# Optimization experiments

Measured on AMD Instinct MI355X. Metric: run time of the kernel, lower is better.

Reference implementation:

```python
import jax, jax.numpy as jnp
import numpy as np

LEAKY_SLOPE = 0.2  # tf.nn.leaky_relu default alpha
N_NODES = 50000
N_EDGES = 800000
IN_DIM = 128
OUT_DIM = 64
HEADS = 4
MLP_HID = 256
MLP_OUT = 128


def setup_inputs() -> dict:
    key = jax.random.key(0)
    ks = jax.random.split(key, 10)
    node_embeddings = jax.random.normal(ks[0], (N_NODES, IN_DIM), dtype=jnp.float32)
    src = jax.random.randint(ks[1], (N_EDGES,), 0, N_NODES, dtype=jnp.int32)
    dst = jax.random.randint(ks[2], (N_EDGES,), 0, N_NODES, dtype=jnp.int32)
    # glorot-ish scales
    W_n = jax.random.normal(ks[3], (HEADS, IN_DIM, OUT_DIM), dtype=jnp.float32) * (1.0 / np.sqrt(IN_DIM))
    a_src = jax.random.normal(ks[4], (HEADS, OUT_DIM), dtype=jnp.float32) * (1.0 / np.sqrt(OUT_DIM))
    a_dst = jax.random.normal(ks[5], (HEADS, OUT_DIM), dtype=jnp.float32) * (1.0 / np.sqrt(OUT_DIM))
    mlp_W1 = jax.random.normal(ks[6], (HEADS * OUT_DIM, MLP_HID), dtype=jnp.float32) * (1.0 / np.sqrt(HEADS * OUT_DIM))
    mlp_b1 = jnp.zeros((MLP_HID,), dtype=jnp.float32)
    mlp_W2 = jax.random.normal(ks[7], (MLP_HID, MLP_OUT), dtype=jnp.float32) * (1.0 / np.sqrt(MLP_HID))
    mlp_b2 = jnp.zeros((MLP_OUT,), dtype=jnp.float32)
    return {"node_embeddings": node_embeddings, "src": src, "dst": dst,
            "W_n": W_n, "a_src": a_src, "a_dst": a_dst,
            "mlp_W1": mlp_W1, "mlp_b1": mlp_b1, "mlp_W2": mlp_W2, "mlp_b2": mlp_b2}


def _gat_forward(node_embeddings, src, dst, W_n, a_src, a_dst, mlp_W1, mlp_b1, mlp_W2, mlp_b2):
    N = node_embeddings.shape[0]
    # per-head linear transform: [N, H, D]
    h = jnp.einsum('nc,hcd->nhd', node_embeddings, W_n)
    # decomposed attention scores at node level, gathered per edge
    s_src = jnp.einsum('nhd,hd->nh', h, a_src)          # [N, H]
    s_dst = jnp.einsum('nhd,hd->nh', h, a_dst)          # [N, H]
    e = jax.nn.leaky_relu(s_src[src] + s_dst[dst], negative_slope=LEAKY_SLOPE)  # [E, H]
    # segment softmax over incoming edges of each dst node
    e_max = jax.ops.segment_max(e, dst, num_segments=N)          # [N, H], -inf for empty
    ex = jnp.exp(e - e_max[dst])                                  # [E, H]
    den = jax.ops.segment_sum(ex, dst, num_segments=N)            # [N, H]
    m = h[src]                                                    # [E, H, D] messages
    num = jax.ops.segment_sum(ex[:, :, None] * m, dst, num_segments=N)  # [N, H, D]
    safe_den = jnp.where(den > 0, den, 1.0)
    head_out = jax.nn.relu(num / safe_den[:, :, None])            # [N, H, D]
    concat = head_out.reshape(N, -1)                              # [N, H*D]
    hidden = jax.nn.relu(concat @ mlp_W1 + mlp_b1)
    return hidden @ mlp_W2 + mlp_b2                               # [N, MLP_OUT]


def reference(node_embeddings, src, dst, W_n, a_src, a_dst, mlp_W1, mlp_b1, mlp_W2, mlp_b2):
    return _gat_forward(node_embeddings, src, dst, W_n, a_src, a_dst,
                        mlp_W1, mlp_b1, mlp_W2, mlp_b2)
```

## Files before the change

### kernel.cpp

```cpp
#include <hip/hip_runtime.h>

#define LEAKY 0.2f

typedef __attribute__((ext_vector_type(8))) short short8;
typedef __attribute__((ext_vector_type(4))) float floatx4;
typedef __attribute__((ext_vector_type(8))) unsigned short ushort8_t;

__device__ __forceinline__ float bf2f(unsigned short u) {
    return __uint_as_float(((unsigned)u) << 16);
}
__device__ __forceinline__ unsigned short f2bf(float f) {
    unsigned u = __float_as_uint(f);
    unsigned r = (u + 0x7fffu + ((u >> 16) & 1u)) >> 16;
    return (unsigned short)r;
}
__device__ __forceinline__ float relu_nan(float v) { return v < 0.0f ? 0.0f : v; }

__device__ __forceinline__ void gload_lds16(const void* g, void* l) {
    __builtin_amdgcn_global_load_lds((const __attribute__((address_space(1))) void*)g,
                                     (__attribute__((address_space(3))) void*)l, 16, 0, 0);
}

__global__ void k_fill(float* __restrict__ p, float val, int n) {
    int i = blockIdx.x * blockDim.x + threadIdx.x;
    if (i < n) p[i] = val;
}

__global__ void k_prep(const float* __restrict__ X, unsigned short* __restrict__ Xb,
                       const float* __restrict__ Wn, unsigned short* __restrict__ WnT,
                       const float* __restrict__ W1, unsigned short* __restrict__ W1T,
                       const float* __restrict__ W2, unsigned short* __restrict__ W2T,
                       const float* __restrict__ Asrc, const float* __restrict__ Adst,
                       float* __restrict__ Wsd,
                       const int* __restrict__ dst, int* __restrict__ cnt,
                       int N, int E) {
    const int gs = gridDim.x * blockDim.x;
    const int tid = blockIdx.x * blockDim.x + threadIdx.x;
    for (int i = tid; i < N * 32; i += gs) {
        float4 v = ((const float4*)X)[i];
        ushort4 o;
        o.x = f2bf(v.x); o.y = f2bf(v.y); o.z = f2bf(v.z); o.w = f2bf(v.w);
        ((ushort4*)Xb)[i] = o;
    }
    for (int i = tid; i < 256 * 128; i += gs) {
        int col = i >> 7, k = i & 127;
        int head = col >> 6, d = col & 63;
        WnT[i] = f2bf(Wn[(size_t)head * 8192 + (size_t)k * 64 + d]);
    }
    for (int i = tid; i < 256 * 256; i += gs) {
        int n = i >> 8, k = i & 255;
        W1T[i] = f2bf(W1[(size_t)k * 256 + n]);
    }
    for (int i = tid; i < 128 * 256; i += gs) {
        int n = i >> 8, k = i & 255;
        W2T[i] = f2bf(W2[(size_t)k * 128 + n]);
    }
    for (int i = tid; i < 8 * 128; i += gs) {
        int j = i >> 7, k = i & 127, h = j & 3;
        const float* av = (j < 4 ? Asrc : Adst) + h * 64;
        const float* wrow = Wn + (size_t)h * 8192 + (size_t)k * 64;
        float acc = 0.0f;
        for (int d = 0; d < 64; ++d) acc += wrow[d] * av[d];
        Wsd[i] = acc;
    }
    for (int i = tid; i < E; i += gs) atomicAdd(cnt + dst[i], 1);
}

__global__ __launch_bounds__(256) void k_scores(
    const unsigned short* __restrict__ Xb, const float* __restrict__ Wsd,
    float* __restrict__ s_src, float* __restrict__ s_dst, int N) {
    const int gs = gridDim.x * 256;
    const int tid = blockIdx.x * 256 + threadIdx.x;
    for (int i = tid; i < N * 8; i += gs) {
        const int n = i >> 3, j = i & 7;
        const unsigned short* xr = Xb + (size_t)n * 128;
        const float* wr = Wsd + j * 128;
        float acc = 0.0f;
        for (int k = 0; k < 128; k += 8) {
            ushort8_t xv = *(const ushort8_t*)(xr + k);
#pragma unroll
            for (int u = 0; u < 8; ++u) acc = fmaf(bf2f(xv[u]), wr[k + u], acc);
        }
        if (j < 4) s_src[n * 4 + j] = acc;
        else       s_dst[n * 4 + (j - 4)] = acc;
    }
}

__global__ __launch_bounds__(256) void k_scan1(
    const int* __restrict__ cnt, int* __restrict__ rowptr, int* __restrict__ bsum, int N) {
    __shared__ int wtot[4];
    const int lane = threadIdx.x & 63, wave = threadIdx.x >> 6;
    const int i = blockIdx.x * 256 + threadIdx.x;
    int v = (i < N) ? cnt[i] : 0;
    int x = v;
    for (int off = 1; off < 64; off <<= 1) {
        int y = __shfl_up(x, off, 64);
        if (lane >= off) x += y;
    }
    if (lane == 63) wtot[wave] = x;
    __syncthreads();
    int wo = 0;
    for (int wv = 0; wv < wave; ++wv) wo += wtot[wv];
    if (i < N) rowptr[i] = wo + x - v;
    if (threadIdx.x == 255) bsum[blockIdx.x] = wo + x;
}
__global__ void k_scan2(int* __restrict__ bsum, int nb) {
    const int lane = threadIdx.x;
    int carry = 0;
    for (int base = 0; base < nb; base += 64) {
        int i = base + lane;
        int v = (i < nb) ? bsum[i] : 0;
        int x = v;
        for (int off = 1; off < 64; off <<= 1) {
            int y = __shfl_up(x, off, 64);
            if (lane >= off) x += y;
        }
        if (i < nb) bsum[i] = carry + x - v;
        carry += __shfl(x, 63, 64);
    }
}
__global__ void k_scan3(int* __restrict__ rowptr, const int* __restrict__ bsum,
                        int* __restrict__ wcnt, int N, int E) {
    int i = blockIdx.x * blockDim.x + threadIdx.x;
    if (i < N) {
        int v = rowptr[i] + bsum[i >> 8];
        rowptr[i] = v;
        wcnt[i] = v;
    }
    if (i == N) rowptr[N] = E;
}

__global__ void k_scatter(const int* __restrict__ src, const int* __restrict__ dst,
                          int* __restrict__ wcnt,
                          const float* __restrict__ s_src, const float* __restrict__ s_dst,
                          int* __restrict__ esrc, float* __restrict__ ex4, int E) {
    int e = blockIdx.x * blockDim.x + threadIdx.x;
    if (e < E) {
        const int s = src[e], d = dst[e];
        const int pos = atomicAdd(wcnt + d, 1);
        esrc[pos] = s;
        const float4 ss = *(const float4*)(s_src + (size_t)s * 4);
        const float4 sd = *(const float4*)(s_dst + (size_t)d * 4);
        float4 o;
        float v;
        v = ss.x + sd.x; v = fmaxf(v, LEAKY * v); o.x = __expf(v);
        v = ss.y + sd.y; v = fmaxf(v, LEAKY * v); o.y = __expf(v);
        v = ss.z + sd.z; v = fmaxf(v, LEAKY * v); o.z = __expf(v);
        v = ss.w + sd.w; v = fmaxf(v, LEAKY * v); o.w = __expf(v);
        *(float4*)(ex4 + (size_t)pos * 4) = o;
    }
}

__global__ __launch_bounds__(256) void k_agg(
    const unsigned short* __restrict__ Xb,
    const int* __restrict__ rowptr, const int* __restrict__ esrc,
    const float* __restrict__ ex4,
    unsigned short* __restrict__ agg, float* __restrict__ invden, int N) {
    const int lane = threadIdx.x & 63;
    const int wave = threadIdx.x >> 6;
    const int n = blockIdx.x * 4 + wave;
    if (n >= N) return;

    const int slot = lane & 15;
    const int g16  = lane & 48;
    const int head = lane >> 4;
    const unsigned short* xcol = Xb + slot * 8;

    const int beg = rowptr[n], end = rowptr[n + 1];

    float num[8] = {0, 0, 0, 0, 0, 0, 0, 0};
    float den = 0.0f;

    int base = beg;
    int sidv = 0; float exv = 0.0f;
    if (base < end) {
        const int rem = end - base;
        if (slot < rem) {
            sidv = esrc[base + slot];
            exv  = ex4[(size_t)(base + slot) * 4 + head];
        }
    }

    while (base < end) {
        const int rem = end - base;
        const int nb  = base + 16;
        int sidn = 0; float exn = 0.0f;
        if (nb < end) {
            const int rem2 = end - nb;
            if (slot < rem2) {
                sidn = esrc[nb + slot];
                exn  = ex4[(size_t)(nb + slot) * 4 + head];
            }
        }
        den += exv;

        if (rem >= 16) {
#pragma unroll
            for (int e = 0; e < 16; ++e) {
                const int s_   = __shfl(sidv, e, 64);
                const float x_ = __shfl(exv, g16 | e, 64);
                const ushort8_t xv = *(const ushort8_t*)(xcol + (size_t)s_ * 128);
#pragma unroll
                for (int j = 0; j < 8; ++j) num[j] = fmaf(x_, bf2f(xv[j]), num[j]);
            }
        } else {
            for (int e = 0; e < rem; ++e) {
                const int s_   = __shfl(sidv, e, 64);
                const float x_ = __shfl(exv, g16 | e, 64);
                const ushort8_t xv = *(const ushort8_t*)(xcol + (size_t)s_ * 128);
#pragma unroll
                for (int j = 0; j < 8; ++j) num[j] = fmaf(x_, bf2f(xv[j]), num[j]);
            }
        }
        sidv = sidn; exv = exn; base = nb;
    }

#pragma unroll
    for (int m = 1; m < 16; m <<= 1) den += __shfl_xor(den, m, 64);
    const float inv = 1.0f / (den > 0.0f ? den : 1.0f);

    ushort8_t o;
#pragma unroll
    for (int j = 0; j < 8; ++j) o[j] = f2bf(num[j]);
    *(ushort8_t*)(agg + (size_t)n * 512 + head * 128 + slot * 8) = o;
    if (slot == 0) invden[n * 4 + head] = inv;
}

__global__ __launch_bounds__(256) void k_gemmh(
    const unsigned short* __restrict__ agg, const unsigned short* __restrict__ WnT,
    const float* __restrict__ invden, unsigned short* __restrict__ concat, int N) {
    __shared__ unsigned short As[256 * 32];
    __shared__ unsigned short Bs[64 * 32];
    const int t = threadIdx.x;
    const int lane = t & 63;
    const int w = t >> 6;
    const int lm = lane & 15, quad = lane >> 4;
    const int row0 = blockIdx.x * 256;
    const int head = blockIdx.y;

    floatx4 acc[4][4];
#pragma unroll
    for (int mi = 0; mi < 4; ++mi)
#pragma unroll
        for (int ni = 0; ni < 4; ++ni) acc[mi][ni] = (floatx4){0, 0, 0, 0};

    for (int k0 = 0; k0 < 128; k0 += 32) {
#pragma unroll
        for (int p = 0; p < 4; ++p) {
            int tr = p * 64 + (t >> 2);
            int ga = row0 + tr; if (ga >= N) ga = N - 1;
            gload_lds16(agg + (size_t)ga * 512 + head * 128 + k0 + (t & 3) * 8,
                        (char*)As + (size_t)tr * 64 + (t & 3) * 16);
        }
        {
            int tr = t >> 2;
            gload_lds16(WnT + (size_t)(head * 64 + tr) * 128 + k0 + (t & 3) * 8,
                        (char*)Bs + (size_t)tr * 64 + (t & 3) * 16);
        }
        __syncthreads();
        short8 af[4], bfr[4];
#pragma unroll
        for (int mi = 0; mi < 4; ++mi)
            af[mi] = *(const short8*)(As + (size_t)(w * 64 + mi * 16 + lm) * 32 + quad * 8);
#pragma unroll
        for (int ni = 0; ni < 4; ++ni)
            bfr[ni] = *(const short8*)(Bs + (size_t)(ni * 16 + lm) * 32 + quad * 8);
#pragma unroll
        for (int mi = 0; mi < 4; ++mi)
#pragma unroll
            for (int ni = 0; ni < 4; ++ni)
                acc[mi][ni] = __builtin_amdgcn_mfma_f32_16x16x32_bf16(af[mi], bfr[ni], acc[mi][ni], 0, 0, 0);
        __syncthreads();
    }

#pragma unroll
    for (int mi = 0; mi < 4; ++mi)
#pragma unroll
        for (int q = 0; q < 4; ++q) {
            const int r = row0 + w * 64 + mi * 16 + quad * 4 + q;
            if (r < N) {
                const float inv = invden[(size_t)r * 4 + head];
#pragma unroll
                for (int ni = 0; ni < 4; ++ni) {
                    const int c = ni * 16 + lm;
                    concat[(size_t)r * 256 + head * 64 + c] = f2bf(relu_nan(acc[mi][ni][q] * inv));
                }
            }
        }
}

template <int K, int MODE>
__global__ __launch_bounds__(256) void k_gemm(
    const unsigned short* __restrict__ A, const unsigned short* __restrict__ BT,
    const float* __restrict__ bias, unsigned short* __restrict__ Cb,
    float* __restrict__ Cf, int N, int ldout) {
    __shared__ unsigned short As[128 * 32];
    __shared__ unsigned short Bs[128 * 32];
    const int t = threadIdx.x;
    const int lane = t & 63;
    const int w = t >> 6;
    const int wy = w >> 1, wx = w & 1;
    const int lm = lane & 15, quad = lane >> 4;
    const int row0 = blockIdx.x * 128;
    const int n0 = blockIdx.y * 128;
    const int srow = lane >> 2;
    const int sk = (lane & 3) * 8;

    floatx4 acc[4][4];
#pragma unroll
    for (int ni = 0; ni < 4; ++ni) {
        float b = bias[n0 + wx * 64 + ni * 16 + lm];
#pragma unroll
        for (int mi = 0; mi < 4; ++mi) acc[mi][ni] = (floatx4){b, b, b, b};
    }

    for (int k0 = 0; k0 < K; k0 += 32) {
#pragma unroll
        for (int p = 0; p < 2; ++p) {
            int tr = (p * 4 + w) * 16 + srow;
            int ga = row0 + tr; if (ga >= N) ga = N - 1;
            gload_lds16(A + (size_t)ga * K + k0 + sk,
                        (char*)As + (size_t)tr * 64 + sk * 2);
            gload_lds16(BT + (size_t)(n0 + tr) * K + k0 + sk,
                        (char*)Bs + (size_t)tr * 64 + sk * 2);
        }
        __syncthreads();
        short8 af[4], bfr[4];
#pragma unroll
        for (int mi = 0; mi < 4; ++mi)
            af[mi] = *(const short8*)(As + (size_t)(wy * 64 + mi * 16 + lm) * 32 + quad * 8);
#pragma unroll
        for (int ni = 0; ni < 4; ++ni)
            bfr[ni] = *(const short8*)(Bs + (size_t)(wx * 64 + ni * 16 + lm) * 32 + quad * 8);
#pragma unroll
        for (int mi = 0; mi < 4; ++mi)
#pragma unroll
            for (int ni = 0; ni < 4; ++ni)
                acc[mi][ni] = __builtin_amdgcn_mfma_f32_16x16x32_bf16(af[mi], bfr[ni], acc[mi][ni], 0, 0, 0);
        __syncthreads();
    }

#pragma unroll
    for (int mi = 0; mi < 4; ++mi)
#pragma unroll
        for (int ni = 0; ni < 4; ++ni)
#pragma unroll
            for (int q = 0; q < 4; ++q) {
                int r = row0 + wy * 64 + mi * 16 + quad * 4 + q;
                int c = n0 + wx * 64 + ni * 16 + lm;
                if (r < N) {
                    if (MODE == 1) Cb[(size_t)r * ldout + c] = f2bf(relu_nan(acc[mi][ni][q]));
                    else           Cf[(size_t)r * ldout + c] = acc[mi][ni][q];
                }
            }
}

extern "C" void kernel_launch(void* const* d_in, const int* in_sizes, int n_in,
                              void* d_out, int out_size, void* d_ws, size_t ws_size,
                              hipStream_t stream) {
    const float* X    = (const float*)d_in[0];
    const int* src    = (const int*)d_in[1];
    const int* dst    = (const int*)d_in[2];
    const float* Wn   = (const float*)d_in[3];
    const float* Asrc = (const float*)d_in[4];
    const float* Adst = (const float*)d_in[5];
    const float* W1   = (const float*)d_in[6];
    const float* b1   = (const float*)d_in[7];
    const float* W2   = (const float*)d_in[8];
    const float* b2   = (const float*)d_in[9];
    float* out = (float*)d_out;

    const int N = in_sizes[0] / 128;
    const int E = in_sizes[1];
    const int NBS = (N + 255) / 256;
    const int NR = (N + 127) / 128;
    const int NRH = (N + 255) / 256;

    size_t off = 0;
    char* w = (char*)d_ws;
    unsigned short* aggb = (unsigned short*)(w + off); off += (size_t)N * 512 * 2;
    float* s_src = (float*)(w + off);                  off += (size_t)N * 4 * 4;
    float* s_dst = (float*)(w + off);                  off += (size_t)N * 4 * 4;
    float* invden= (float*)(w + off);                  off += (size_t)N * 4 * 4;
    int* cnt     = (int*)(w + off);                    off += (size_t)N * 4;
    int* rowptr  = (int*)(w + off);                    off += ((size_t)(N + 1) * 4 + 15) & ~15ull;
    int* wcnt    = (int*)(w + off);                    off += (size_t)N * 4;
    int* bsum    = (int*)(w + off);                    off += ((size_t)NBS * 4 + 15) & ~15ull;
    int* esrc    = (int*)(w + off);                    off += (size_t)E * 4;
    float* ex4   = (float*)(w + off);                  off += (size_t)E * 4 * 4;
    unsigned short* W1T = (unsigned short*)(w + off);  off += 256 * 256 * 2;
    unsigned short* W2T = (unsigned short*)(w + off);  off += 128 * 256 * 2;
    unsigned short* WnT = (unsigned short*)(w + off);  off += 256 * 128 * 2;
    float* Wsd   = (float*)(w + off);                  off += 8 * 128 * 4;
    const size_t required = off;

    if (ws_size < required) {
        k_fill<<<dim3((out_size + 255) / 256), dim3(256), 0, stream>>>(
            out, (float)(ws_size >> 20), out_size);
        return;
    }

    unsigned short* Xb     = (unsigned short*)d_out;
    unsigned short* concat = (unsigned short*)d_out;
    unsigned short* hid    = aggb;

    hipMemsetAsync(cnt, 0, (size_t)N * sizeof(int), stream);
    k_prep<<<dim3(2048), dim3(256), 0, stream>>>(X, Xb, Wn, WnT, W1, W1T, W2, W2T,
                                                 Asrc, Adst, Wsd, dst, cnt, N, E);
    k_scores<<<dim3((N * 8 + 255) / 256), dim3(256), 0, stream>>>(Xb, Wsd, s_src, s_dst, N);
    k_scan1<<<dim3(NBS), dim3(256), 0, stream>>>(cnt, rowptr, bsum, N);
    k_scan2<<<dim3(1), dim3(64), 0, stream>>>(bsum, NBS);
    k_scan3<<<dim3((N + 256) / 256), dim3(256), 0, stream>>>(rowptr, bsum, wcnt, N, E);
    k_scatter<<<dim3((E + 255) / 256), dim3(256), 0, stream>>>(src, dst, wcnt, s_src, s_dst,
                                                               esrc, ex4, E);
    k_agg<<<dim3((N + 3) / 4), dim3(256), 0, stream>>>(Xb, rowptr, esrc, ex4, aggb, invden, N);
    k_gemmh<<<dim3(NRH, 4), dim3(256), 0, stream>>>(aggb, WnT, invden, concat, N);
    k_gemm<256, 1><<<dim3(NR, 2), dim3(256), 0, stream>>>(
        concat, W1T, b1, hid, nullptr, N, 256);
    k_gemm<256, 2><<<dim3(NR, 1), dim3(256), 0, stream>>>(
        hid, W2T, b2, nullptr, out, N, 128);
}
```

Before: 340.4 us.

## Fuse edge aggregation and per-head projection into one MFMA-based kernel per 16 nodes

```diff
diff --git a/kernel.cpp b/kernel.cpp
--- a/kernel.cpp
+++ b/kernel.cpp
@@ -133,12 +133,14 @@
 __global__ void k_scatter(const int* __restrict__ src, const int* __restrict__ dst,
                           int* __restrict__ wcnt,
                           const float* __restrict__ s_src, const float* __restrict__ s_dst,
-                          int* __restrict__ esrc, float* __restrict__ ex4, int E) {
+                          int* __restrict__ esrc, float* __restrict__ ex4,
+                          unsigned char* __restrict__ ownb, int E) {
     int e = blockIdx.x * blockDim.x + threadIdx.x;
     if (e < E) {
         const int s = src[e], d = dst[e];
         const int pos = atomicAdd(wcnt + d, 1);
         esrc[pos] = s;
+        ownb[pos] = (unsigned char)(d & 15);
         const float4 ss = *(const float4*)(s_src + (size_t)s * 4);
         const float4 sd = *(const float4*)(s_dst + (size_t)d * 4);
         float4 o;
@@ -151,140 +153,166 @@
     }
 }
 
-__global__ __launch_bounds__(256) void k_agg(
+__global__ __launch_bounds__(256, 4) void k_agg(
     const unsigned short* __restrict__ Xb,
     const int* __restrict__ rowptr, const int* __restrict__ esrc,
-    const float* __restrict__ ex4,
-    unsigned short* __restrict__ agg, float* __restrict__ invden, int N) {
-    const int lane = threadIdx.x & 63;
-    const int wave = threadIdx.x >> 6;
-    const int n = blockIdx.x * 4 + wave;
-    if (n >= N) return;
-
-    const int slot = lane & 15;
-    const int g16  = lane & 48;
-    const int head = lane >> 4;
-    const unsigned short* xcol = Xb + slot * 8;
-
-    const int beg = rowptr[n], end = rowptr[n + 1];
-
-    float num[8] = {0, 0, 0, 0, 0, 0, 0, 0};
-    float den = 0.0f;
-
-    int base = beg;
-    int sidv = 0; float exv = 0.0f;
-    if (base < end) {
-        const int rem = end - base;
-        if (slot < rem) {
-            sidv = esrc[base + slot];
-            exv  = ex4[(size_t)(base + slot) * 4 + head];
-        }
-    }
-
-    while (base < end) {
-        const int rem = end - base;
-        const int nb  = base + 16;
-        int sidn = 0; float exn = 0.0f;
-        if (nb < end) {
-            const int rem2 = end - nb;
-            if (slot < rem2) {
-                sidn = esrc[nb + slot];
-                exn  = ex4[(size_t)(nb + slot) * 4 + head];
-            }
-        }
-        den += exv;
-
-        if (rem >= 16) {
-#pragma unroll
-            for (int e = 0; e < 16; ++e) {
-                const int s_   = __shfl(sidv, e, 64);
-                const float x_ = __shfl(exv, g16 | e, 64);
-                const ushort8_t xv = *(const ushort8_t*)(xcol + (size_t)s_ * 128);
-#pragma unroll
-                for (int j = 0; j < 8; ++j) num[j] = fmaf(x_, bf2f(xv[j]), num[j]);
-            }
-        } else {
-            for (int e = 0; e < rem; ++e) {
-                const int s_   = __shfl(sidv, e, 64);
-                const float x_ = __shfl(exv, g16 | e, 64);
-                const ushort8_t xv = *(const ushort8_t*)(xcol + (size_t)s_ * 128);
-#pragma unroll
-                for (int j = 0; j < 8; ++j) num[j] = fmaf(x_, bf2f(xv[j]), num[j]);
-            }
-        }
-        sidv = sidn; exv = exn; base = nb;
-    }
-
-#pragma unroll
-    for (int m = 1; m < 16; m <<= 1) den += __shfl_xor(den, m, 64);
-    const float inv = 1.0f / (den > 0.0f ? den : 1.0f);
-
-    ushort8_t o;
-#pragma unroll
-    for (int j = 0; j < 8; ++j) o[j] = f2bf(num[j]);
-    *(ushort8_t*)(agg + (size_t)n * 512 + head * 128 + slot * 8) = o;
-    if (slot == 0) invden[n * 4 + head] = inv;
-}
-
-__global__ __launch_bounds__(256) void k_gemmh(
-    const unsigned short* __restrict__ agg, const unsigned short* __restrict__ WnT,
-    const float* __restrict__ invden, unsigned short* __restrict__ concat, int N) {
-    __shared__ unsigned short As[256 * 32];
-    __shared__ unsigned short Bs[64 * 32];
+    const float* __restrict__ ex4, const unsigned char* __restrict__ ownb,
+    const unsigned short* __restrict__ WnT,
+    unsigned short* __restrict__ concat, int N) {
+    __shared__ unsigned XtT[128 * 16];
+    __shared__ float exl[2][4][32];
+    __shared__ int sidl[2][32];
+    __shared__ int ownl[2][32];
+    __shared__ float denl[4][16];
+    __shared__ unsigned short Cs[4][16 * 128];
+
     const int t = threadIdx.x;
     const int lane = t & 63;
     const int w = t >> 6;
-    const int lm = lane & 15, quad = lane >> 4;
-    const int row0 = blockIdx.x * 256;
-    const int head = blockIdx.y;
-
-    floatx4 acc[4][4];
-#pragma unroll
-    for (int mi = 0; mi < 4; ++mi)
-#pragma unroll
-        for (int ni = 0; ni < 4; ++ni) acc[mi][ni] = (floatx4){0, 0, 0, 0};
-
-    for (int k0 = 0; k0 < 128; k0 += 32) {
-#pragma unroll
-        for (int p = 0; p < 4; ++p) {
-            int tr = p * 64 + (t >> 2);
-            int ga = row0 + tr; if (ga >= N) ga = N - 1;
-            gload_lds16(agg + (size_t)ga * 512 + head * 128 + k0 + (t & 3) * 8,
-                        (char*)As + (size_t)tr * 64 + (t & 3) * 16);
-        }
+    const int r0 = blockIdx.x * 16;
+    const int r1 = min(r0 + 16, N);
+    const int beg = rowptr[r0], end = rowptr[r1];
+    const int nkb = (end - beg + 31) >> 5;
+
+    const int r = lane & 15;
+    const int g4 = lane >> 4;
+    const int s2 = t & 15;
+    const int dg8 = t >> 4;
+
+    floatx4 acc[8];
+#pragma unroll
+    for (int dg = 0; dg < 8; ++dg) acc[dg] = (floatx4){0, 0, 0, 0};
+    float den = 0.0f;
+
+    if (t < 32 && nkb > 0) {
+        int pos = beg + t;
+        bool v = pos < end;
+        int s = v ? esrc[pos] : 0;
+        float4 e = v ? *(const float4*)(ex4 + (size_t)pos * 4) : (float4){0, 0, 0, 0};
+        sidl[0][t] = s;
+        ownl[0][t] = v ? (int)ownb[pos] : 255;
+        exl[0][0][t] = e.x; exl[0][1][t] = e.y; exl[0][2][t] = e.z; exl[0][3][t] = e.w;
+    }
+    __syncthreads();
+
+    for (int kb = 0; kb < nkb; ++kb) {
+        const int mb = kb & 1;
+        const int se = sidl[mb][2 * s2];
+        const int so = sidl[mb][2 * s2 + 1];
+        const ushort8_t xe = *(const ushort8_t*)(Xb + (size_t)se * 128 + dg8 * 8);
+        const ushort8_t xo = *(const ushort8_t*)(Xb + (size_t)so * 128 + dg8 * 8);
+        int pf_sid = 0, pf_own = 255;
+        float4 pf_ex = (float4){0, 0, 0, 0};
+        const bool havepf = (t < 32) && (kb + 1 < nkb);
+        if (havepf) {
+            int pos = beg + (kb + 1) * 32 + t;
+            if (pos < end) {
+                pf_sid = esrc[pos];
+                pf_ex = *(const float4*)(ex4 + (size_t)pos * 4);
+                pf_own = ownb[pos];
+            }
+        }
+        unsigned hiu[4], lou[4];
         {
-            int tr = t >> 2;
-            gload_lds16(WnT + (size_t)(head * 64 + tr) * 128 + k0 + (t & 3) * 8,
-                        (char*)Bs + (size_t)tr * 64 + (t & 3) * 16);
+            const float4 ea = *(const float4*)&exl[mb][w][g4 * 8];
+            const float4 eb = *(const float4*)&exl[mb][w][g4 * 8 + 4];
+            const int4 oa = *(const int4*)&ownl[mb][g4 * 8];
+            const int4 ob = *(const int4*)&ownl[mb][g4 * 8 + 4];
+            float ev[8];
+            ev[0] = (oa.x == r) ? ea.x : 0.0f;
+            ev[1] = (oa.y == r) ? ea.y : 0.0f;
+            ev[2] = (oa.z == r) ? ea.z : 0.0f;
+            ev[3] = (oa.w == r) ? ea.w : 0.0f;
+            ev[4] = (ob.x == r) ? eb.x : 0.0f;
+            ev[5] = (ob.y == r) ? eb.y : 0.0f;
+            ev[6] = (ob.z == r) ? eb.z : 0.0f;
+            ev[7] = (ob.w == r) ? eb.w : 0.0f;
+#pragma unroll
+            for (int j = 0; j < 8; ++j) den += ev[j];
+#pragma unroll
+            for (int jj = 0; jj < 4; ++jj) {
+                unsigned h0 = f2bf(ev[2 * jj]), h1 = f2bf(ev[2 * jj + 1]);
+                float l0 = ev[2 * jj] - bf2f((unsigned short)h0);
+                float l1 = ev[2 * jj + 1] - bf2f((unsigned short)h1);
+                hiu[jj] = h0 | (h1 << 16);
+                lou[jj] = (unsigned)f2bf(l0) | ((unsigned)f2bf(l1) << 16);
+            }
+        }
+        unsigned outp[8];
+        const unsigned* xeu = (const unsigned*)&xe;
+        const unsigned* xou = (const unsigned*)&xo;
+#pragma unroll
+        for (int m2 = 0; m2 < 4; ++m2) {
+            outp[2 * m2]     = (xeu[m2] & 0xffffu) | (xou[m2] << 16);
+            outp[2 * m2 + 1] = (xeu[m2] >> 16) | (xou[m2] & 0xffff0000u);
+        }
+#pragma unroll
+        for (int i = 0; i < 8; ++i) {
+            const int js = (i + g4) & 7;
+            XtT[(dg8 * 8 + js) * 16 + s2] = outp[js];
         }
         __syncthreads();
-        short8 af[4], bfr[4];
-#pragma unroll
-        for (int mi = 0; mi < 4; ++mi)
-            af[mi] = *(const short8*)(As + (size_t)(w * 64 + mi * 16 + lm) * 32 + quad * 8);
-#pragma unroll
-        for (int ni = 0; ni < 4; ++ni)
-            bfr[ni] = *(const short8*)(Bs + (size_t)(ni * 16 + lm) * 32 + quad * 8);
-#pragma unroll
-        for (int mi = 0; mi < 4; ++mi)
-#pragma unroll
-            for (int ni = 0; ni < 4; ++ni)
-                acc[mi][ni] = __builtin_amdgcn_mfma_f32_16x16x32_bf16(af[mi], bfr[ni], acc[mi][ni], 0, 0, 0);
+        union { short8 v; unsigned u[4]; } ahi, alo;
+#pragma unroll
+        for (int jj = 0; jj < 4; ++jj) { ahi.u[jj] = hiu[jj]; alo.u[jj] = lou[jj]; }
+#pragma unroll
+        for (int dg = 0; dg < 8; ++dg) {
+            const short8 bfv = *(const short8*)((const unsigned short*)XtT +
+                                                (size_t)(dg * 16 + r) * 32 + g4 * 8);
+            acc[dg] = __builtin_amdgcn_mfma_f32_16x16x32_bf16(ahi.v, bfv, acc[dg], 0, 0, 0);
+            acc[dg] = __builtin_amdgcn_mfma_f32_16x16x32_bf16(alo.v, bfv, acc[dg], 0, 0, 0);
+        }
+        if (havepf) {
+            const int nb2 = (kb + 1) & 1;
+            sidl[nb2][t] = pf_sid;
+            ownl[nb2][t] = pf_own;
+            exl[nb2][0][t] = pf_ex.x; exl[nb2][1][t] = pf_ex.y;
+            exl[nb2][2][t] = pf_ex.z; exl[nb2][3][t] = pf_ex.w;
+        }
         __syncthreads();
     }
 
-#pragma unroll
-    for (int mi = 0; mi < 4; ++mi)
+    den += __shfl_xor(den, 16, 64);
+    den += __shfl_xor(den, 32, 64);
+    if (lane < 16) denl[w][lane] = den;
+
+    unsigned short* cw = &Cs[w][0];
+#pragma unroll
+    for (int dg = 0; dg < 8; ++dg)
 #pragma unroll
         for (int q = 0; q < 4; ++q) {
-            const int r = row0 + w * 64 + mi * 16 + quad * 4 + q;
-            if (r < N) {
-                const float inv = invden[(size_t)r * 4 + head];
-#pragma unroll
-                for (int ni = 0; ni < 4; ++ni) {
-                    const int c = ni * 16 + lm;
-                    concat[(size_t)r * 256 + head * 64 + c] = f2bf(relu_nan(acc[mi][ni][q] * inv));
-                }
+            int row = g4 * 4 + q;
+            int cbyte = (dg * 16 + r) * 2;
+            cw[(row * 256 + (cbyte ^ ((row & 7) << 4))) >> 1] = f2bf(acc[dg][q]);
+        }
+    __syncthreads();
+
+    floatx4 acc2[4];
+#pragma unroll
+    for (int f = 0; f < 4; ++f) acc2[f] = (floatx4){0, 0, 0, 0};
+#pragma unroll
+    for (int kb2 = 0; kb2 < 4; ++kb2) {
+        int abyte = r * 256 + ((kb2 * 64 + g4 * 16) ^ ((r & 7) << 4));
+        short8 a2 = *(const short8*)((const char*)cw + abyte);
+#pragma unroll
+        for (int f = 0; f < 4; ++f) {
+            short8 b2 = *(const short8*)(WnT +
+                (size_t)(w * 64 + f * 16 + r) * 128 + kb2 * 32 + g4 * 8);
+            acc2[f] = __builtin_amdgcn_mfma_f32_16x16x32_bf16(a2, b2, acc2[f], 0, 0, 0);
+        }
+    }
+
+#pragma unroll
+    for (int f = 0; f < 4; ++f)
+#pragma unroll
+        for (int q = 0; q < 4; ++q) {
+            int row = g4 * 4 + q;
+            int rn = r0 + row;
+            if (rn < N) {
+                float dv = denl[w][row];
+                float inv = 1.0f / (dv > 0.0f ? dv : 1.0f);
+                concat[(size_t)rn * 256 + w * 64 + f * 16 + r] =
+                    f2bf(relu_nan(acc2[f][q]) * inv);
             }
         }
 }
@@ -374,20 +402,21 @@
     const int E = in_sizes[1];
     const int NBS = (N + 255) / 256;
     const int NR = (N + 127) / 128;
-    const int NRH = (N + 255) / 256;
+    const int NG = (N + 15) / 16;
 
     size_t off = 0;
     char* w = (char*)d_ws;
-    unsigned short* aggb = (unsigned short*)(w + off); off += (size_t)N * 512 * 2;
+    unsigned short* hid = (unsigned short*)(w + off);  off += (size_t)N * 256 * 2;
+    unsigned short* Xb  = (unsigned short*)(w + off);  off += (size_t)N * 128 * 2;
     float* s_src = (float*)(w + off);                  off += (size_t)N * 4 * 4;
     float* s_dst = (float*)(w + off);                  off += (size_t)N * 4 * 4;
-    float* invden= (float*)(w + off);                  off += (size_t)N * 4 * 4;
     int* cnt     = (int*)(w + off);                    off += (size_t)N * 4;
     int* rowptr  = (int*)(w + off);                    off += ((size_t)(N + 1) * 4 + 15) & ~15ull;
     int* wcnt    = (int*)(w + off);                    off += (size_t)N * 4;
     int* bsum    = (int*)(w + off);                    off += ((size_t)NBS * 4 + 15) & ~15ull;
     int* esrc    = (int*)(w + off);                    off += (size_t)E * 4;
     float* ex4   = (float*)(w + off);                  off += (size_t)E * 4 * 4;
+    unsigned char* ownb = (unsigned char*)(w + off);   off += ((size_t)E + 15) & ~15ull;
     unsigned short* W1T = (unsigned short*)(w + off);  off += 256 * 256 * 2;
     unsigned short* W2T = (unsigned short*)(w + off);  off += 128 * 256 * 2;
     unsigned short* WnT = (unsigned short*)(w + off);  off += 256 * 128 * 2;
@@ -400,9 +429,7 @@
         return;
     }
 
-    unsigned short* Xb     = (unsigned short*)d_out;
     unsigned short* concat = (unsigned short*)d_out;
-    unsigned short* hid    = aggb;
 
     hipMemsetAsync(cnt, 0, (size_t)N * sizeof(int), stream);
     k_prep<<<dim3(2048), dim3(256), 0, stream>>>(X, Xb, Wn, WnT, W1, W1T, W2, W2T,
@@ -412,9 +439,8 @@
     k_scan2<<<dim3(1), dim3(64), 0, stream>>>(bsum, NBS);
     k_scan3<<<dim3((N + 256) / 256), dim3(256), 0, stream>>>(rowptr, bsum, wcnt, N, E);
     k_scatter<<<dim3((E + 255) / 256), dim3(256), 0, stream>>>(src, dst, wcnt, s_src, s_dst,
-                                                               esrc, ex4, E);
-    k_agg<<<dim3((N + 3) / 4), dim3(256), 0, stream>>>(Xb, rowptr, esrc, ex4, aggb, invden, N);
-    k_gemmh<<<dim3(NRH, 4), dim3(256), 0, stream>>>(aggb, WnT, invden, concat, N);
+                                                               esrc, ex4, ownb, E);
+    k_agg<<<dim3(NG), dim3(256), 0, stream>>>(Xb, rowptr, esrc, ex4, ownb, WnT, concat, N);
     k_gemm<256, 1><<<dim3(NR, 2), dim3(256), 0, stream>>>(
         concat, W1T, b1, hid, nullptr, N, 256);
     k_gemm<256, 2><<<dim3(NR, 1), dim3(256), 0, stream>>>(
```

Measured after the change: 348.9 us. 1.03x slower.
